# Kernel tuning notes

Measured on AMD Instinct MI355X. Metric: run time of the kernel, lower is better.

The kernel has to match this reference:

```python
import jax, jax.numpy as jnp
import numpy as np

SPATIAL_DIM = 2
N_IN = 4096
N_OUT = 1024
C_IN = 32
C_OUT = 32
FILTER_SEQ = (64, 64)
BATCH = 16


def _grid(num_points):
    # replicates: meshgrid(indexing='xy') of linspace(0,1,n) per dim, dstack, view(-1, d)
    n = int(num_points ** (1.0 / SPATIAL_DIM))
    nodes = np.linspace(0.0, 1.0, n)
    X, Y = np.meshgrid(nodes, nodes, indexing='xy')
    return np.dstack((X, Y)).reshape(-1, SPATIAL_DIM)  # (n^2, 2)


def _cache():
    # replicates QuadConvLayer.cache(): bump-support sparsity pattern
    out_locs = _grid(N_OUT)               # (N_OUT, 2)
    in_nodes = _grid(N_IN)                # (N_IN, 2)
    locs = out_locs[:, None, :] - in_nodes[None, :, :]   # (N_OUT, N_IN, 2)
    bump_arg = np.linalg.norm(locs, axis=2) ** 4
    decay_param = (N_IN / 16.0) ** 2
    mask = bump_arg <= 1.0 / decay_param
    idx = np.argwhere(mask)               # (E, 2), row-major sorted like torch.nonzero
    eval_locs = locs[mask]                # (E, 2)
    return eval_locs.astype(np.float32), idx.astype(np.int64)


def setup_inputs() -> dict:
    key = jax.random.key(0)
    k_feat, k1, k2, k3 = jax.random.split(key, 4)
    eval_locs, eval_indices = _cache()
    # filter MLP G: Linear(2,64,bias=False) -> Sin -> Linear(64,64) -> Sin -> Linear(64, C_IN*C_OUT)
    d0, d1, d2, d3 = SPATIAL_DIM, FILTER_SEQ[0], FILTER_SEQ[1], C_IN * C_OUT
    W1 = jax.random.normal(k1, (d0, d1), jnp.float32) / np.sqrt(d0)
    W2 = jax.random.normal(k2, (d1, d2), jnp.float32) / np.sqrt(d1)
    W3 = jax.random.normal(k3, (d2, d3), jnp.float32) / np.sqrt(d2)
    features = jax.random.normal(k_feat, (BATCH, C_IN, N_IN), jnp.float32)
    return {
        "features": features,
        "W1": W1,
        "W2": W2,
        "W3": W3,
        "eval_locs": jnp.asarray(eval_locs),
        "eval_indices": jnp.asarray(eval_indices),
    }


def reference(features, W1, W2, W3, eval_locs, eval_indices):
    B = features.shape[0]
    E = eval_locs.shape[0]
    seg = eval_indices[:, 0]   # output point per edge (sorted)
    src = eval_indices[:, 1]   # input point per edge
    # filter MLP with Sin activations: (E, 2) -> (E, C_IN, C_OUT)
    h = jnp.sin(eval_locs @ W1)
    h = jnp.sin(h @ W2)
    filt = (h @ W3).reshape(E, C_IN, C_OUT)
    # gather features at source points: (B, C_IN, E)
    gathered = features[:, :, src]
    # faithful to torch: a raw reshape (NOT a transpose) of (B, C_IN, E) -> (B, E, C_IN)
    g = gathered.reshape(B, E, C_IN)
    vals = jnp.einsum('bni,nij->bnj', g, filt)   # (B, E, C_OUT)
    # faithful raw reshape (B, E, C_OUT) -> (B, C_OUT, E)
    vals = vals.reshape(B, C_OUT, E)
    # scatter-sum over edges into output points (segment_coo sum)
    integral = jnp.zeros((B, C_OUT, N_OUT), features.dtype).at[:, :, seg].add(vals)
    return integral
```

## Files before the change

### kernel.cpp

```cpp
#include <hip/hip_runtime.h>
#include <hip/hip_bf16.h>

typedef __bf16 bf16x8  __attribute__((ext_vector_type(8)));
typedef __bf16 bf16x16 __attribute__((ext_vector_type(16)));
typedef float  f32x4   __attribute__((ext_vector_type(4)));

#define N_IN   4096
#define N_OUT  1024
#define BATCH  16
#define ROWS   16

#define H1_STR   72
#define H2_STR   72
#define FT_JSTR  40
#define FTH_NSTR 640
#define G_STR    520
#define V_STR    520

#define WS_W3T_OFF    0
#define WS_W2T_OFF    131072
#define WS_FEATT_OFF  139264
#define WS_NEED       4333568

__global__ void qc_zero_kernel(float* __restrict__ out, int n4) {
    int i = blockIdx.x * blockDim.x + threadIdx.x;
    if (i < n4) ((float4*)out)[i] = make_float4(0.f, 0.f, 0.f, 0.f);
}

__global__ void qc_prep_kernel(const float* __restrict__ w3, const float* __restrict__ w2,
                               __bf16* __restrict__ w3t, __bf16* __restrict__ w2t) {
    int gid = blockIdx.x * blockDim.x + threadIdx.x;
    if (gid < 65536) {
        int k = gid & 63, col = gid >> 6;
        w3t[gid] = (__bf16)w3[k * 1024 + col];
    } else {
        int j = gid - 65536;
        int k = j & 63, col = j >> 6;
        w2t[j] = (__bf16)w2[k * 64 + col];
    }
}

__global__ void qc_prep2_kernel(const float* __restrict__ w3, const float* __restrict__ w2,
                                const float* __restrict__ feat,
                                float* __restrict__ out,
                                __bf16* __restrict__ w3t, __bf16* __restrict__ w2t,
                                __bf16* __restrict__ featT) {
    int bid = blockIdx.x, tid = threadIdx.x;
    if (bid < 512) {
        int i = bid * 256 + tid;
        ((float4*)out)[i] = make_float4(0.f, 0.f, 0.f, 0.f);
    } else if (bid < 768) {
        int gid = (bid - 512) * 256 + tid;
        int k = gid & 63, col = gid >> 6;
        w3t[gid] = (__bf16)w3[k * 1024 + col];
    } else if (bid < 784) {
        int j = (bid - 768) * 256 + tid;
        int k = j & 63, col = j >> 6;
        w2t[j] = (__bf16)w2[k * 64 + col];
    } else {
        int bid2 = bid - 784;
        int c    = bid2 >> 4;
        int src  = (bid2 & 15) * 256 + tid;
        bf16x16 v;
        #pragma unroll
        for (int b = 0; b < 16; ++b)
            v[b] = (__bf16)feat[(b * 32 + c) * N_IN + src];
        __bf16* p = &featT[((size_t)c * N_IN + src) * 16];
        *(bf16x8*)p       = *(bf16x8*)&v;
        *(bf16x8*)(p + 8) = *((bf16x8*)&v + 1);
    }
}

__global__ __launch_bounds__(512, 6)
void qc_fused_kernel(const __bf16* __restrict__ featT,
                     const float* __restrict__ w1,
                     const float* __restrict__ locs,
                     const int*   __restrict__ eidx,
                     const __bf16* __restrict__ w2t,
                     const __bf16* __restrict__ w3t,
                     float* __restrict__ out,
                     int E)
{
    __shared__ __align__(16) __bf16 h1b[ROWS * H1_STR];
    __shared__ __align__(16) __bf16 h2b[ROWS * H2_STR];
    __shared__ __align__(16) __bf16 ftv[ROWS * FTH_NSTR];
    __shared__ __align__(16) __bf16 gb [BATCH * G_STR];
    __shared__ unsigned short seg_s[512];

    const int tid = threadIdx.x;
    const int n0  = blockIdx.x * ROWS;
    const int t0  = n0 * 32;
    const int ch0 = t0 / E;
    const int m0  = t0 - ch0 * E;

    int mm = m0 + tid;
    const int cc = ch0 + (mm >= E);
    if (mm >= E) mm -= E;
    int2 p = ((const int2*)eidx)[mm];
    bf16x16 gv = {};
    if (cc < 32)
        gv = *(const bf16x16*)&featT[((size_t)cc * N_IN + p.y) * 16];
    seg_s[tid] = (unsigned short)p.x;

    {
        const int r  = tid >> 5;
        const int j0 = (tid & 31) * 2;
        float lx = 0.f, ly = 0.f;
        int n = n0 + r;
        if (n < E) { lx = locs[n * 2]; ly = locs[n * 2 + 1]; }
        float2 wa = *(const float2*)&w1[j0];
        float2 wb = *(const float2*)&w1[64 + j0];
        __bf16* h = &h1b[r * H1_STR + j0];
        h[0] = (__bf16)__sinf(lx * wa.x + ly * wb.x);
        h[1] = (__bf16)__sinf(lx * wa.y + ly * wb.y);
    }
    __syncthreads();

    const int lane = tid & 63;
    const int wv   = tid >> 6;
    const int ml   = lane & 15;
    const int q    = lane >> 4;

    if (wv < 4) {
        bf16x8 a0 = *(const bf16x8*)&h1b[ml * H1_STR + q * 8];
        bf16x8 a1 = *(const bf16x8*)&h1b[ml * H1_STR + 32 + q * 8];
        const __bf16* wp = &w2t[(wv * 16 + ml) * 64 + q * 8];
        bf16x8 b0 = *(const bf16x8*)wp;
        bf16x8 b1 = *(const bf16x8*)(wp + 32);
        f32x4 c = {0.f, 0.f, 0.f, 0.f};
        c = __builtin_amdgcn_mfma_f32_16x16x32_bf16(a0, b0, c, 0, 0, 0);
        c = __builtin_amdgcn_mfma_f32_16x16x32_bf16(a1, b1, c, 0, 0, 0);
        #pragma unroll
        for (int g_ = 0; g_ < 4; ++g_)
            h2b[(q * 4 + g_) * H2_STR + wv * 16 + ml] = (__bf16)__sinf(c[g_]);
    }
    __syncthreads();

    #pragma unroll
    for (int b = 0; b < 16; ++b)
        gb[b * G_STR + tid] = gv[b];

    bf16x8 ha0 = *(const bf16x8*)&h2b[ml * H2_STR + q * 8];
    bf16x8 ha1 = *(const bf16x8*)&h2b[ml * H2_STR + 32 + q * 8];

    bf16x8 ag[2];
    f32x4  c0[2], c1[2];

    #pragma unroll
    for (int tt = 0; tt < 4; ++tt) {
        int i_  = wv * 4 + tt;
        int col = i_ * 32 + ml;
        const __bf16* wp = &w3t[col * 64 + q * 8];
        bf16x8 b0 = *(const bf16x8*)wp;
        bf16x8 b1 = *(const bf16x8*)(wp + 32);
        f32x4 c = {0.f, 0.f, 0.f, 0.f};
        c = __builtin_amdgcn_mfma_f32_16x16x32_bf16(ha0, b0, c, 0, 0, 0);
        c = __builtin_amdgcn_mfma_f32_16x16x32_bf16(ha1, b1, c, 0, 0, 0);
        __bf16* fp = &ftv[ml * FT_JSTR + i_];
        fp[(q * 4 + 0) * FTH_NSTR] = (__bf16)c[0];
        fp[(q * 4 + 1) * FTH_NSTR] = (__bf16)c[1];
        fp[(q * 4 + 2) * FTH_NSTR] = (__bf16)c[2];
        fp[(q * 4 + 3) * FTH_NSTR] = (__bf16)c[3];
    }
    __syncthreads();

    {
        bf16x8 f0[2];
        #pragma unroll
        for (int rr = 0; rr < 2; ++rr) {
            int r = wv * 2 + rr;
            f0[rr] = *(const bf16x8*)&ftv[r * FTH_NSTR + ml * FT_JSTR + q * 8];
            ag[rr] = *(const bf16x8*)&gb[ml * G_STR + r * 32 + q * 8];
        }
        #pragma unroll
        for (int rr = 0; rr < 2; ++rr) {
            f32x4 z = {0.f, 0.f, 0.f, 0.f};
            c0[rr] = __builtin_amdgcn_mfma_f32_16x16x32_bf16(ag[rr], f0[rr], z, 0, 0, 0);
        }
    }
    __syncthreads();

    #pragma unroll
    for (int tt = 0; tt < 4; ++tt) {
        int i_  = wv * 4 + tt;
        int col = i_ * 32 + 16 + ml;
        const __bf16* wp = &w3t[col * 64 + q * 8];
        bf16x8 b0 = *(const bf16x8*)wp;
        bf16x8 b1 = *(const bf16x8*)(wp + 32);
        f32x4 c = {0.f, 0.f, 0.f, 0.f};
        c = __builtin_amdgcn_mfma_f32_16x16x32_bf16(ha0, b0, c, 0, 0, 0);
        c = __builtin_amdgcn_mfma_f32_16x16x32_bf16(ha1, b1, c, 0, 0, 0);
        __bf16* fp = &ftv[ml * FT_JSTR + i_];
        fp[(q * 4 + 0) * FTH_NSTR] = (__bf16)c[0];
        fp[(q * 4 + 1) * FTH_NSTR] = (__bf16)c[1];
        fp[(q * 4 + 2) * FTH_NSTR] = (__bf16)c[2];
        fp[(q * 4 + 3) * FTH_NSTR] = (__bf16)c[3];
    }
    __syncthreads();

    {
        bf16x8 f1[2];
        #pragma unroll
        for (int rr = 0; rr < 2; ++rr) {
            int r = wv * 2 + rr;
            f1[rr] = *(const bf16x8*)&ftv[r * FTH_NSTR + ml * FT_JSTR + q * 8];
        }
        #pragma unroll
        for (int rr = 0; rr < 2; ++rr) {
            f32x4 z = {0.f, 0.f, 0.f, 0.f};
            c1[rr] = __builtin_amdgcn_mfma_f32_16x16x32_bf16(ag[rr], f1[rr], z, 0, 0, 0);
        }
        __bf16* valsb = gb;
        #pragma unroll
        for (int rr = 0; rr < 2; ++rr) {
            int r = wv * 2 + rr;
            __bf16* vp = &valsb[r * 32];
            #pragma unroll
            for (int g_ = 0; g_ < 4; ++g_) {
                int b = q * 4 + g_;
                vp[b * V_STR + ml]      = (__bf16)c0[rr][g_];
                vp[b * V_STR + 16 + ml] = (__bf16)c1[rr][g_];
            }
        }
    }
    __syncthreads();

    {
        const __bf16* valsb = gb;
        const int b    = tid >> 5;
        const int rem  = tid & 31;
        const int tl0  = (rem >> 1) * 32 + (rem & 1) * 16;
        const __bf16* vp = &valsb[b * V_STR + tl0];
        bf16x8 v0 = *(const bf16x8*)(vp);
        bf16x8 v1 = *(const bf16x8*)(vp + 8);
        float vv[16];
        #pragma unroll
        for (int j = 0; j < 8; ++j) { vv[j] = (float)v0[j]; vv[8 + j] = (float)v1[j]; }
        int key_prev = -1;
        float acc = 0.f;
        #pragma unroll
        for (int j = 0; j < 16; ++j) {
            int mm2 = m0 + tl0 + j;
            int cc2 = ch0 + (mm2 >= E);
            if (mm2 >= E) mm2 -= E;
            if (cc2 < 32) {
                int o   = (int)seg_s[tl0 + j];
                int key = ((b * 32 + cc2) << 10) | o;
                if (key != key_prev) {
                    if (key_prev >= 0) atomicAdd(&out[key_prev], acc);
                    key_prev = key;
                    acc = vv[j];
                } else {
                    acc += vv[j];
                }
            }
        }
        if (key_prev >= 0) atomicAdd(&out[key_prev], acc);
    }
}

#define FB_FT_NSTR 1288
__global__ __launch_bounds__(256, 2)
void qc_main_kernel(const float* __restrict__ feat,
                    const float* __restrict__ w1,
                    const float* __restrict__ w2,
                    const float* __restrict__ locs,
                    const int*   __restrict__ eidx,
                    const __bf16* __restrict__ w3t,
                    float* __restrict__ out,
                    int E)
{
    __shared__ __align__(16) __bf16 h1b[ROWS * H1_STR];
    __shared__ __align__(16) __bf16 h2b[ROWS * H2_STR];
    __shared__ __align__(16) __bf16 ftv[ROWS * FB_FT_NSTR];
    __shared__ __align__(16) __bf16 gb [BATCH * G_STR];
    __shared__ unsigned short seg_s[512];
    __shared__ unsigned short src_s[512];

    const int tid = threadIdx.x;
    const int n0  = blockIdx.x * ROWS;
    const int t0  = n0 * 32;
    const int ch0 = t0 / E;
    const int m0  = t0 - ch0 * E;

    {
        const int r  = tid >> 4;
        const int j0 = (tid & 15) * 4;
        float lx = 0.f, ly = 0.f;
        int n = n0 + r;
        if (n < E) { lx = locs[n * 2]; ly = locs[n * 2 + 1]; }
        float4 wa = *(const float4*)&w1[j0];
        float4 wb = *(const float4*)&w1[64 + j0];
        __bf16* h = &h1b[r * H1_STR + j0];
        h[0] = (__bf16)__sinf(lx * wa.x + ly * wb.x);
        h[1] = (__bf16)__sinf(lx * wa.y + ly * wb.y);
        h[2] = (__bf16)__sinf(lx * wa.z + ly * wb.z);
        h[3] = (__bf16)__sinf(lx * wa.w + ly * wb.w);
    }
    for (int tl = tid; tl < 512; tl += 256) {
        int mm = m0 + tl; if (mm >= E) mm -= E;
        seg_s[tl] = (unsigned short)eidx[mm * 2];
        src_s[tl] = (unsigned short)eidx[mm * 2 + 1];
    }
    __syncthreads();

    {
        const int r  = tid >> 4;
        const int j0 = (tid & 15) * 4;
        float a0 = 0.f, a1 = 0.f, a2 = 0.f, a3 = 0.f;
        const __bf16* h1r = &h1b[r * H1_STR];
        #pragma unroll 8
        for (int k = 0; k < 64; ++k) {
            float h = (float)h1r[k];
            float4 w = *(const float4*)&w2[k * 64 + j0];
            a0 += h * w.x; a1 += h * w.y; a2 += h * w.z; a3 += h * w.w;
        }
        __bf16* h = &h2b[r * H2_STR + j0];
        h[0] = (__bf16)__sinf(a0);
        h[1] = (__bf16)__sinf(a1);
        h[2] = (__bf16)__sinf(a2);
        h[3] = (__bf16)__sinf(a3);
    }
    #pragma unroll 4
    for (int it = 0; it < 32; ++it) {
        int idx = it * 256 + tid;
        int b   = idx >> 9;
        int tl  = idx & 511;
        int mm  = m0 + tl;
        int cc  = ch0 + (mm >= E);
        if (mm >= E) mm -= E;
        float v = 0.f;
        if (cc < 32) v = feat[(b * 32 + cc) * N_IN + (int)src_s[tl]];
        gb[b * G_STR + tl] = (__bf16)v;
    }
    __syncthreads();

    const int lane = tid & 63;
    const int wv   = tid >> 6;
    const int ml   = lane & 15;
    const int q    = lane >> 4;

    {
        bf16x8 a0 = *(const bf16x8*)&h2b[ml * H2_STR + q * 8];
        bf16x8 a1 = *(const bf16x8*)&h2b[ml * H2_STR + 32 + q * 8];
        #pragma unroll
        for (int t = 0; t < 16; ++t) {
            int col = wv * 256 + t * 16 + ml;
            const __bf16* wp = &w3t[col * 64 + q * 8];
            bf16x8 b0 = *(const bf16x8*)wp;
            bf16x8 b1 = *(const bf16x8*)(wp + 32);
            f32x4 c = {0.f, 0.f, 0.f, 0.f};
            c = __builtin_amdgcn_mfma_f32_16x16x32_bf16(a0, b0, c, 0, 0, 0);
            c = __builtin_amdgcn_mfma_f32_16x16x32_bf16(a1, b1, c, 0, 0, 0);
            int i_ = col >> 5, j_ = col & 31;
            __bf16* fp = &ftv[j_ * FT_JSTR + i_];
            fp[(q * 4 + 0) * FB_FT_NSTR] = (__bf16)c[0];
            fp[(q * 4 + 1) * FB_FT_NSTR] = (__bf16)c[1];
            fp[(q * 4 + 2) * FB_FT_NSTR] = (__bf16)c[2];
            fp[(q * 4 + 3) * FB_FT_NSTR] = (__bf16)c[3];
        }
    }
    __syncthreads();

    {
        bf16x8 ag[4], f0[4], f1[4];
        #pragma unroll
        for (int rr = 0; rr < 4; ++rr) {
            int r = wv * 4 + rr;
            ag[rr] = *(const bf16x8*)&gb[ml * G_STR + r * 32 + q * 8];
            f0[rr] = *(const bf16x8*)&ftv[r * FB_FT_NSTR + ml        * FT_JSTR + q * 8];
            f1[rr] = *(const bf16x8*)&ftv[r * FB_FT_NSTR + (16 + ml) * FT_JSTR + q * 8];
        }
        __syncthreads();
        __bf16* valsb = ftv;
        #pragma unroll
        for (int rr = 0; rr < 4; ++rr) {
            int r = wv * 4 + rr;
            f32x4 c0 = {0.f, 0.f, 0.f, 0.f};
            f32x4 c1 = {0.f, 0.f, 0.f, 0.f};
            c0 = __builtin_amdgcn_mfma_f32_16x16x32_bf16(ag[rr], f0[rr], c0, 0, 0, 0);
            c1 = __builtin_amdgcn_mfma_f32_16x16x32_bf16(ag[rr], f1[rr], c1, 0, 0, 0);
            __bf16* vp = &valsb[r * 32];
            #pragma unroll
            for (int g_ = 0; g_ < 4; ++g_) {
                int b = q * 4 + g_;
                vp[b * V_STR + ml]      = (__bf16)c0[g_];
                vp[b * V_STR + 16 + ml] = (__bf16)c1[g_];
            }
        }
    }
    __syncthreads();

    {
        const __bf16* valsb = ftv;
        const int b = tid >> 4;
        const int r = tid & 15;
        const __bf16* vp = &valsb[b * V_STR + r * 32];
        bf16x8 v0 = *(const bf16x8*)(vp);
        bf16x8 v1 = *(const bf16x8*)(vp + 8);
        bf16x8 v2 = *(const bf16x8*)(vp + 16);
        bf16x8 v3 = *(const bf16x8*)(vp + 24);
        float vv[32];
        #pragma unroll
        for (int j = 0; j < 8; ++j) {
            vv[j]      = (float)v0[j];
            vv[8 + j]  = (float)v1[j];
            vv[16 + j] = (float)v2[j];
            vv[24 + j] = (float)v3[j];
        }
        const int tl0 = r * 32;
        int key_prev = -1;
        float acc = 0.f;
        #pragma unroll
        for (int j = 0; j < 32; ++j) {
            int mm = m0 + tl0 + j;
            int cc = ch0 + (mm >= E);
            if (mm >= E) mm -= E;
            if (cc < 32) {
                int o   = (int)seg_s[tl0 + j];
                int key = ((b * 32 + cc) << 10) | o;
                if (key != key_prev) {
                    if (key_prev >= 0) atomicAdd(&out[key_prev], acc);
                    key_prev = key;
                    acc = vv[j];
                } else {
                    acc += vv[j];
                }
            }
        }
        if (key_prev >= 0) atomicAdd(&out[key_prev], acc);
    }
}

extern "C" void kernel_launch(void* const* d_in, const int* in_sizes, int n_in,
                              void* d_out, int out_size, void* d_ws, size_t ws_size,
                              hipStream_t stream)
{
    (void)n_in;
    const float* feat = (const float*)d_in[0];
    const float* w1   = (const float*)d_in[1];
    const float* w2   = (const float*)d_in[2];
    const float* w3   = (const float*)d_in[3];
    const float* locs = (const float*)d_in[4];
    const int*   eidx = (const int*)d_in[5];
    float* out  = (float*)d_out;

    const int E = in_sizes[4] / 2;
    if (E <= 0) return;

    __bf16* w3t   = (__bf16*)((char*)d_ws + WS_W3T_OFF);
    __bf16* w2t   = (__bf16*)((char*)d_ws + WS_W2T_OFF);
    __bf16* featT = (__bf16*)((char*)d_ws + WS_FEATT_OFF);

    int nblocks = (E + ROWS - 1) / ROWS;

    if (ws_size >= (size_t)WS_NEED) {
        qc_prep2_kernel<<<1296, 256, 0, stream>>>(w3, w2, feat, out, w3t, w2t, featT);
        qc_fused_kernel<<<nblocks, 512, 0, stream>>>(featT, w1, locs, eidx, w2t, w3t, out, E);
    } else {
        int n4 = out_size / 4;
        qc_zero_kernel<<<(n4 + 255) / 256, 256, 0, stream>>>(out, n4);
        qc_prep_kernel<<<272, 256, 0, stream>>>(w3, w2, w3t, w2t);
        qc_main_kernel<<<nblocks, 256, 0, stream>>>(feat, w1, w2, locs, eidx, w3t, out, E);
    }
}
```

Baseline: 150.9 us.

## Process 32 edges per block in fused kernel with aliased shared buffers

Doubles the rows per block from 16 to 32, so each W3 B-fragment loaded from global feeds two MFMAs (two row groups) and W3 traffic per edge is halved. Shared memory for gather, filter and vals buffers is aliased into one region, and the scatter phase handles 32 consecutive elements per thread, which can merge more runs before each atomicAdd. The block count halves and extra syncs are added to protect the aliased buffer. Launch bounds drop to 2 blocks per CU, which may lower occupancy.

```diff
diff --git a/kernel.cpp b/kernel.cpp
--- a/kernel.cpp
+++ b/kernel.cpp
@@ -16,6 +16,7 @@
 #define FTH_NSTR 640
 #define G_STR    520
 #define V_STR    520
+#define GSTR2    1032
 
 #define WS_W3T_OFF    0
 #define WS_W2T_OFF    131072
@@ -71,48 +72,62 @@
     }
 }
 
-__global__ __launch_bounds__(512, 6)
-void qc_fused_kernel(const __bf16* __restrict__ featT,
-                     const float* __restrict__ w1,
-                     const float* __restrict__ locs,
-                     const int*   __restrict__ eidx,
-                     const __bf16* __restrict__ w2t,
-                     const __bf16* __restrict__ w3t,
-                     float* __restrict__ out,
-                     int E)
+__global__ __launch_bounds__(512, 2)
+void qc_fused32_kernel(const __bf16* __restrict__ featT,
+                       const float* __restrict__ w1,
+                       const float* __restrict__ locs,
+                       const int*   __restrict__ eidx,
+                       const __bf16* __restrict__ w2t,
+                       const __bf16* __restrict__ w3t,
+                       float* __restrict__ out,
+                       int E)
 {
-    __shared__ __align__(16) __bf16 h1b[ROWS * H1_STR];
-    __shared__ __align__(16) __bf16 h2b[ROWS * H2_STR];
-    __shared__ __align__(16) __bf16 ftv[ROWS * FTH_NSTR];
-    __shared__ __align__(16) __bf16 gb [BATCH * G_STR];
-    __shared__ unsigned short seg_s[512];
+    __shared__ __align__(16) unsigned char region1[40960];
+    __shared__ __align__(16) __bf16 h1b[32 * H1_STR];
+    __shared__ __align__(16) __bf16 h2b[32 * H2_STR];
+    __shared__ unsigned short seg_s[1024];
+
+    __bf16* gb   = (__bf16*)region1;
+    __bf16* ftv  = (__bf16*)region1;
+    __bf16* vals = (__bf16*)region1;
 
     const int tid = threadIdx.x;
-    const int n0  = blockIdx.x * ROWS;
+    const int n0  = blockIdx.x * 32;
     const int t0  = n0 * 32;
     const int ch0 = t0 / E;
     const int m0  = t0 - ch0 * E;
 
-    int mm = m0 + tid;
-    const int cc = ch0 + (mm >= E);
-    if (mm >= E) mm -= E;
-    int2 p = ((const int2*)eidx)[mm];
-    bf16x16 gv = {};
-    if (cc < 32)
-        gv = *(const bf16x16*)&featT[((size_t)cc * N_IN + p.y) * 16];
-    seg_s[tid] = (unsigned short)p.x;
-
-    {
-        const int r  = tid >> 5;
-        const int j0 = (tid & 31) * 2;
+    bf16x16 gvv[2];
+    #pragma unroll
+    for (int h = 0; h < 2; ++h) {
+        int tl = tid + h * 512;
+        int mm = m0 + tl;
+        int cc = ch0 + (mm >= E);
+        if (mm >= E) mm -= E;
+        int2 p = ((const int2*)eidx)[mm];
+        seg_s[tl] = (unsigned short)p.x;
+        int ccc = cc < 32 ? cc : 31;
+        bf16x16 g = *(const bf16x16*)&featT[((size_t)ccc * N_IN + p.y) * 16];
+        if (cc >= 32) {
+            #pragma unroll
+            for (int z = 0; z < 16; ++z) g[z] = (__bf16)0.f;
+        }
+        gvv[h] = g;
+    }
+
+    {
+        const int r  = tid >> 4;
+        const int j0 = (tid & 15) * 4;
         float lx = 0.f, ly = 0.f;
         int n = n0 + r;
         if (n < E) { lx = locs[n * 2]; ly = locs[n * 2 + 1]; }
-        float2 wa = *(const float2*)&w1[j0];
-        float2 wb = *(const float2*)&w1[64 + j0];
-        __bf16* h = &h1b[r * H1_STR + j0];
-        h[0] = (__bf16)__sinf(lx * wa.x + ly * wb.x);
-        h[1] = (__bf16)__sinf(lx * wa.y + ly * wb.y);
+        float4 wa = *(const float4*)&w1[j0];
+        float4 wb = *(const float4*)&w1[64 + j0];
+        __bf16* hp = &h1b[r * H1_STR + j0];
+        hp[0] = (__bf16)__sinf(lx * wa.x + ly * wb.x);
+        hp[1] = (__bf16)__sinf(lx * wa.y + ly * wb.y);
+        hp[2] = (__bf16)__sinf(lx * wa.z + ly * wb.z);
+        hp[3] = (__bf16)__sinf(lx * wa.w + ly * wb.w);
     }
     __syncthreads();
 
@@ -121,10 +136,12 @@
     const int ml   = lane & 15;
     const int q    = lane >> 4;
 
-    if (wv < 4) {
-        bf16x8 a0 = *(const bf16x8*)&h1b[ml * H1_STR + q * 8];
-        bf16x8 a1 = *(const bf16x8*)&h1b[ml * H1_STR + 32 + q * 8];
-        const __bf16* wp = &w2t[(wv * 16 + ml) * 64 + q * 8];
+    {
+        const int rg = (wv >> 2) * 16;
+        const int cw = (wv & 3) * 16;
+        bf16x8 a0 = *(const bf16x8*)&h1b[(rg + ml) * H1_STR + q * 8];
+        bf16x8 a1 = *(const bf16x8*)&h1b[(rg + ml) * H1_STR + 32 + q * 8];
+        const __bf16* wp = &w2t[(cw + ml) * 64 + q * 8];
         bf16x8 b0 = *(const bf16x8*)wp;
         bf16x8 b1 = *(const bf16x8*)(wp + 32);
         f32x4 c = {0.f, 0.f, 0.f, 0.f};
@@ -132,19 +149,28 @@
         c = __builtin_amdgcn_mfma_f32_16x16x32_bf16(a1, b1, c, 0, 0, 0);
         #pragma unroll
         for (int g_ = 0; g_ < 4; ++g_)
-            h2b[(q * 4 + g_) * H2_STR + wv * 16 + ml] = (__bf16)__sinf(c[g_]);
-    }
-    __syncthreads();
-
-    #pragma unroll
-    for (int b = 0; b < 16; ++b)
-        gb[b * G_STR + tid] = gv[b];
-
-    bf16x8 ha0 = *(const bf16x8*)&h2b[ml * H2_STR + q * 8];
-    bf16x8 ha1 = *(const bf16x8*)&h2b[ml * H2_STR + 32 + q * 8];
-
-    bf16x8 ag[2];
-    f32x4  c0[2], c1[2];
+            h2b[(rg + q * 4 + g_) * H2_STR + cw + ml] = (__bf16)__sinf(c[g_]);
+    }
+    __syncthreads();
+
+    #pragma unroll
+    for (int b = 0; b < 16; ++b) {
+        gb[b * GSTR2 + tid]       = gvv[0][b];
+        gb[b * GSTR2 + 512 + tid] = gvv[1][b];
+    }
+    __syncthreads();
+
+    bf16x8 ag[4];
+    #pragma unroll
+    for (int rr = 0; rr < 4; ++rr)
+        ag[rr] = *(const bf16x8*)&gb[ml * GSTR2 + (wv * 4 + rr) * 32 + q * 8];
+    bf16x8 ha00 = *(const bf16x8*)&h2b[ml * H2_STR + q * 8];
+    bf16x8 ha01 = *(const bf16x8*)&h2b[ml * H2_STR + 32 + q * 8];
+    bf16x8 ha10 = *(const bf16x8*)&h2b[(16 + ml) * H2_STR + q * 8];
+    bf16x8 ha11 = *(const bf16x8*)&h2b[(16 + ml) * H2_STR + 32 + q * 8];
+    __syncthreads();
+
+    f32x4 c0[4], c1[4];
 
     #pragma unroll
     for (int tt = 0; tt < 4; ++tt) {
@@ -153,29 +179,30 @@
         const __bf16* wp = &w3t[col * 64 + q * 8];
         bf16x8 b0 = *(const bf16x8*)wp;
         bf16x8 b1 = *(const bf16x8*)(wp + 32);
-        f32x4 c = {0.f, 0.f, 0.f, 0.f};
-        c = __builtin_amdgcn_mfma_f32_16x16x32_bf16(ha0, b0, c, 0, 0, 0);
-        c = __builtin_amdgcn_mfma_f32_16x16x32_bf16(ha1, b1, c, 0, 0, 0);
+        f32x4 cA = {0.f, 0.f, 0.f, 0.f};
+        f32x4 cB = {0.f, 0.f, 0.f, 0.f};
+        cA = __builtin_amdgcn_mfma_f32_16x16x32_bf16(ha00, b0, cA, 0, 0, 0);
+        cA = __builtin_amdgcn_mfma_f32_16x16x32_bf16(ha01, b1, cA, 0, 0, 0);
+        cB = __builtin_amdgcn_mfma_f32_16x16x32_bf16(ha10, b0, cB, 0, 0, 0);
+        cB = __builtin_amdgcn_mfma_f32_16x16x32_bf16(ha11, b1, cB, 0, 0, 0);
         __bf16* fp = &ftv[ml * FT_JSTR + i_];
-        fp[(q * 4 + 0) * FTH_NSTR] = (__bf16)c[0];
-        fp[(q * 4 + 1) * FTH_NSTR] = (__bf16)c[1];
-        fp[(q * 4 + 2) * FTH_NSTR] = (__bf16)c[2];
-        fp[(q * 4 + 3) * FTH_NSTR] = (__bf16)c[3];
-    }
-    __syncthreads();
-
-    {
-        bf16x8 f0[2];
-        #pragma unroll
-        for (int rr = 0; rr < 2; ++rr) {
-            int r = wv * 2 + rr;
-            f0[rr] = *(const bf16x8*)&ftv[r * FTH_NSTR + ml * FT_JSTR + q * 8];
-            ag[rr] = *(const bf16x8*)&gb[ml * G_STR + r * 32 + q * 8];
-        }
-        #pragma unroll
-        for (int rr = 0; rr < 2; ++rr) {
+        #pragma unroll
+        for (int g_ = 0; g_ < 4; ++g_) {
+            fp[(q * 4 + g_) * FTH_NSTR]        = (__bf16)cA[g_];
+            fp[(16 + q * 4 + g_) * FTH_NSTR]   = (__bf16)cB[g_];
+        }
+    }
+    __syncthreads();
+
+    {
+        bf16x8 f[4];
+        #pragma unroll
+        for (int rr = 0; rr < 4; ++rr)
+            f[rr] = *(const bf16x8*)&ftv[(wv * 4 + rr) * FTH_NSTR + ml * FT_JSTR + q * 8];
+        #pragma unroll
+        for (int rr = 0; rr < 4; ++rr) {
             f32x4 z = {0.f, 0.f, 0.f, 0.f};
-            c0[rr] = __builtin_amdgcn_mfma_f32_16x16x32_bf16(ag[rr], f0[rr], z, 0, 0, 0);
+            c0[rr] = __builtin_amdgcn_mfma_f32_16x16x32_bf16(ag[rr], f[rr], z, 0, 0, 0);
         }
     }
     __syncthreads();
@@ -187,67 +214,72 @@
         const __bf16* wp = &w3t[col * 64 + q * 8];
         bf16x8 b0 = *(const bf16x8*)wp;
         bf16x8 b1 = *(const bf16x8*)(wp + 32);
-        f32x4 c = {0.f, 0.f, 0.f, 0.f};
-        c = __builtin_amdgcn_mfma_f32_16x16x32_bf16(ha0, b0, c, 0, 0, 0);
-        c = __builtin_amdgcn_mfma_f32_16x16x32_bf16(ha1, b1, c, 0, 0, 0);
+        f32x4 cA = {0.f, 0.f, 0.f, 0.f};
+        f32x4 cB = {0.f, 0.f, 0.f, 0.f};
+        cA = __builtin_amdgcn_mfma_f32_16x16x32_bf16(ha00, b0, cA, 0, 0, 0);
+        cA = __builtin_amdgcn_mfma_f32_16x16x32_bf16(ha01, b1, cA, 0, 0, 0);
+        cB = __builtin_amdgcn_mfma_f32_16x16x32_bf16(ha10, b0, cB, 0, 0, 0);
+        cB = __builtin_amdgcn_mfma_f32_16x16x32_bf16(ha11, b1, cB, 0, 0, 0);
         __bf16* fp = &ftv[ml * FT_JSTR + i_];
-        fp[(q * 4 + 0) * FTH_NSTR] = (__bf16)c[0];
-        fp[(q * 4 + 1) * FTH_NSTR] = (__bf16)c[1];
-        fp[(q * 4 + 2) * FTH_NSTR] = (__bf16)c[2];
-        fp[(q * 4 + 3) * FTH_NSTR] = (__bf16)c[3];
-    }
-    __syncthreads();
-
-    {
-        bf16x8 f1[2];
-        #pragma unroll
-        for (int rr = 0; rr < 2; ++rr) {
-            int r = wv * 2 + rr;
-            f1[rr] = *(const bf16x8*)&ftv[r * FTH_NSTR + ml * FT_JSTR + q * 8];
-        }
-        #pragma unroll
-        for (int rr = 0; rr < 2; ++rr) {
-            f32x4 z = {0.f, 0.f, 0.f, 0.f};
-            c1[rr] = __builtin_amdgcn_mfma_f32_16x16x32_bf16(ag[rr], f1[rr], z, 0, 0, 0);
-        }
-        __bf16* valsb = gb;
-        #pragma unroll
-        for (int rr = 0; rr < 2; ++rr) {
-            int r = wv * 2 + rr;
-            __bf16* vp = &valsb[r * 32];
-            #pragma unroll
-            for (int g_ = 0; g_ < 4; ++g_) {
-                int b = q * 4 + g_;
-                vp[b * V_STR + ml]      = (__bf16)c0[rr][g_];
-                vp[b * V_STR + 16 + ml] = (__bf16)c1[rr][g_];
-            }
-        }
-    }
-    __syncthreads();
-
-    {
-        const __bf16* valsb = gb;
-        const int b    = tid >> 5;
-        const int rem  = tid & 31;
-        const int tl0  = (rem >> 1) * 32 + (rem & 1) * 16;
-        const __bf16* vp = &valsb[b * V_STR + tl0];
+        #pragma unroll
+        for (int g_ = 0; g_ < 4; ++g_) {
+            fp[(q * 4 + g_) * FTH_NSTR]        = (__bf16)cA[g_];
+            fp[(16 + q * 4 + g_) * FTH_NSTR]   = (__bf16)cB[g_];
+        }
+    }
+    __syncthreads();
+
+    bf16x8 f1[4];
+    #pragma unroll
+    for (int rr = 0; rr < 4; ++rr)
+        f1[rr] = *(const bf16x8*)&ftv[(wv * 4 + rr) * FTH_NSTR + ml * FT_JSTR + q * 8];
+    __syncthreads();
+    #pragma unroll
+    for (int rr = 0; rr < 4; ++rr) {
+        f32x4 z = {0.f, 0.f, 0.f, 0.f};
+        c1[rr] = __builtin_amdgcn_mfma_f32_16x16x32_bf16(ag[rr], f1[rr], z, 0, 0, 0);
+    }
+    #pragma unroll
+    for (int rr = 0; rr < 4; ++rr) {
+        int r = wv * 4 + rr;
+        __bf16* vp = &vals[r * 32];
+        #pragma unroll
+        for (int g_ = 0; g_ < 4; ++g_) {
+            int b = q * 4 + g_;
+            vp[b * GSTR2 + ml]      = (__bf16)c0[rr][g_];
+            vp[b * GSTR2 + 16 + ml] = (__bf16)c1[rr][g_];
+        }
+    }
+    __syncthreads();
+
+    {
+        const int b   = tid >> 5;
+        const int w   = tid & 31;
+        const int tl0 = w * 32;
+        const __bf16* vp = &vals[b * GSTR2 + tl0];
         bf16x8 v0 = *(const bf16x8*)(vp);
         bf16x8 v1 = *(const bf16x8*)(vp + 8);
-        float vv[16];
-        #pragma unroll
-        for (int j = 0; j < 8; ++j) { vv[j] = (float)v0[j]; vv[8 + j] = (float)v1[j]; }
+        bf16x8 v2 = *(const bf16x8*)(vp + 16);
+        bf16x8 v3 = *(const bf16x8*)(vp + 24);
+        float vv[32];
+        #pragma unroll
+        for (int j = 0; j < 8; ++j) {
+            vv[j]      = (float)v0[j];
+            vv[8 + j]  = (float)v1[j];
+            vv[16 + j] = (float)v2[j];
+            vv[24 + j] = (float)v3[j];
+        }
         int key_prev = -1;
         float acc = 0.f;
         #pragma unroll
-        for (int j = 0; j < 16; ++j) {
+        for (int j = 0; j < 32; ++j) {
             int mm2 = m0 + tl0 + j;
             int cc2 = ch0 + (mm2 >= E);
-            if (mm2 >= E) mm2 -= E;
             if (cc2 < 32) {
                 int o   = (int)seg_s[tl0 + j];
-                int key = ((b * 32 + cc2) << 10) | o;
+                int key = (cc2 << 10) | o;
                 if (key != key_prev) {
-                    if (key_prev >= 0) atomicAdd(&out[key_prev], acc);
+                    if (key_prev >= 0) atomicAdd(&out[(b << 15) + key_prev], acc);
                     key_prev = key;
                     acc = vv[j];
                 } else {
@@ -255,7 +287,7 @@
                 }
             }
         }
-        if (key_prev >= 0) atomicAdd(&out[key_prev], acc);
+        if (key_prev >= 0) atomicAdd(&out[(b << 15) + key_prev], acc);
     }
 }
 
@@ -452,13 +484,13 @@
     __bf16* w2t   = (__bf16*)((char*)d_ws + WS_W2T_OFF);
     __bf16* featT = (__bf16*)((char*)d_ws + WS_FEATT_OFF);
 
-    int nblocks = (E + ROWS - 1) / ROWS;
-
     if (ws_size >= (size_t)WS_NEED) {
+        int nblocks = (E + 31) / 32;
         qc_prep2_kernel<<<1296, 256, 0, stream>>>(w3, w2, feat, out, w3t, w2t, featT);
-        qc_fused_kernel<<<nblocks, 512, 0, stream>>>(featT, w1, locs, eidx, w2t, w3t, out, E);
+        qc_fused32_kernel<<<nblocks, 512, 0, stream>>>(featT, w1, locs, eidx, w2t, w3t, out, E);
     } else {
         int n4 = out_size / 4;
+        int nblocks = (E + ROWS - 1) / ROWS;
         qc_zero_kernel<<<(n4 + 255) / 256, 256, 0, stream>>>(out, n4);
         qc_prep_kernel<<<272, 256, 0, stream>>>(w3, w2, w3t, w2t);
         qc_main_kernel<<<nblocks, 256, 0, stream>>>(feat, w1, w2, locs, eidx, w3t, out, E);
```

Result: faster. 136.5 us (-9.6%).
